# Kernel optimization log

Hardware: AMD Instinct MI355X
Metric: run time of the kernel (lower is better)

The kernel has to match this reference:

```python
import jax, jax.numpy as jnp
from jax import lax
import numpy as np

H = 512       # nhidden
IN = 300      # title/body input dim
TLEN = 40     # title_len
BLEN = 200    # body_len
B = 256       # batch
CH = 512      # classify_hidden
NC = 4        # nclass


def setup_inputs():
    key = jax.random.key(0)
    ks = jax.random.split(key, 17)
    s = 1.0 / np.sqrt(H)
    u = lambda k, sh: jax.random.uniform(k, sh, jnp.float32, -s, s)
    return {
        "x": jax.random.normal(ks[0], (B, TLEN + BLEN, IN), jnp.float32),
        "title_Wih": u(ks[1], (2, 4 * H, IN)),
        "title_Whh": u(ks[2], (2, 4 * H, H)),
        "title_bih": u(ks[3], (2, 4 * H)),
        "title_bhh": u(ks[4], (2, 4 * H)),
        "body_Wih": u(ks[5], (2, 4 * H, IN)),
        "body_Whh": u(ks[6], (2, 4 * H, H)),
        "body_bih": u(ks[7], (2, 4 * H)),
        "body_bhh": u(ks[8], (2, 4 * H)),
        "bil_W": u(ks[9], (1, 2 * H, 2 * H)),
        "bil_b": u(ks[10], (1,)),
        "attn_W": u(ks[11], (2 * H, 4 * H)),
        "attn_b": u(ks[12], (2 * H,)),
        "dec_W": u(ks[13], (CH, 4 * H)),
        "dec_b": u(ks[14], (CH,)),
        "cls_W": u(ks[15], (NC, CH)),
        "cls_b": u(ks[16], (NC,)),
    }


def _lstm_dir(x, Wih, Whh, bih, bhh, h0, c0, reverse):
    # x: [B, T, I]; precompute input-to-gate contributions for all timesteps
    xg = jnp.einsum('bti,gi->btg', x, Wih) + bih + bhh  # [B, T, 4H]

    def step(carry, xg_t):
        h, c = carry
        g = xg_t + h @ Whh.T  # PyTorch gate order: i, f, g, o
        i, f, gg, o = jnp.split(g, 4, axis=-1)
        c = jax.nn.sigmoid(f) * c + jax.nn.sigmoid(i) * jnp.tanh(gg)
        h = jax.nn.sigmoid(o) * jnp.tanh(c)
        return (h, c), h

    (hT, cT), hs = lax.scan(step, (h0, c0), jnp.swapaxes(xg, 0, 1), reverse=reverse)
    return jnp.swapaxes(hs, 0, 1), hT, cT  # outputs aligned to input time order


def _bilstm(x, Wih, Whh, bih, bhh, h0, c0):
    # h0, c0: [2, B, H] (dir 0 = forward, dir 1 = backward)
    out_f, hf, cf = _lstm_dir(x, Wih[0], Whh[0], bih[0], bhh[0], h0[0], c0[0], False)
    out_b, hb, cb = _lstm_dir(x, Wih[1], Whh[1], bih[1], bhh[1], h0[1], c0[1], True)
    out = jnp.concatenate([out_f, out_b], axis=-1)  # [B, T, 2H]
    return out, jnp.stack([hf, hb]), jnp.stack([cf, cb])


def reference(x, title_Wih, title_Whh, title_bih, title_bhh,
              body_Wih, body_Whh, body_bih, body_bhh,
              bil_W, bil_b, attn_W, attn_b, dec_W, dec_b, cls_W, cls_b):
    title, body = x[:, :TLEN, :], x[:, TLEN:, :]
    z = jnp.zeros((2, x.shape[0], H), x.dtype)
    title_out, hn, cn = _bilstm(title, title_Wih, title_Whh, title_bih, title_bhh, z, z)
    # conditional=True: body RNN starts from title final (h, c)
    body_out, _, _ = _bilstm(body, body_Wih, body_Whh, body_bih, body_bhh, hn, cn)
    body_last = body_out[:, -1, :]  # [B, 2H]
    # vectorized bilinear attention over title timesteps (replaces per-t loop)
    scores = jnp.einsum('bte,oeh,bh->bto', title_out, bil_W, body_last) + bil_b
    scores = jax.nn.softmax(scores[..., 0], axis=-1)  # [B, TLEN]
    context = jnp.einsum('bte,bt->be', title_out, scores)  # [B, 2H]
    attn = jnp.tanh(jnp.concatenate([context, body_last], axis=1) @ attn_W.T + attn_b)
    output = jnp.concatenate([title_out[:, -1, :], attn], axis=1)  # [B, 4H]
    class_hidden = output @ dec_W.T + dec_b  # dropout p=0.0 -> identity
    return jax.nn.softmax(class_hidden @ cls_W.T + cls_b, axis=-1)
```

## Files before the change

kernel.cpp:

```cpp
#include <hip/hip_runtime.h>
#include <math.h>

#define HD    512
#define BATCH 256
#define TDIM  240
#define INDIM 300

typedef unsigned short u16;
typedef u16   u16x8 __attribute__((ext_vector_type(8)));
typedef float f32x4 __attribute__((ext_vector_type(4)));

__device__ __forceinline__ u16 bf16_rte(float v) {
    unsigned u = __builtin_bit_cast(unsigned, v);
    unsigned r = (u + 0x7FFFu + ((u >> 16) & 1u)) >> 16;
    return (u16)r;
}

__device__ __forceinline__ void mfma16(f32x4& d, u16x8 a, u16x8 b) {
    asm("v_mfma_f32_16x16x32_bf16 %0, %1, %2, %0" : "+v"(d) : "v"(a), "v"(b));
}

__global__ __launch_bounds__(256) void split_pad(
    const float* __restrict__ src, u16* __restrict__ hi, u16* __restrict__ lo,
    int rows, int kin, int kout)
{
    long i = (long)blockIdx.x * 256 + threadIdx.x;
    if (i >= (long)rows * kout) return;
    int r = (int)(i / kout);
    int k = (int)(i - (long)r * kout);
    float v = (k < kin) ? src[(long)r * kin + k] : 0.f;
    u16 h = bf16_rte(v);
    float hf = __builtin_bit_cast(float, (unsigned)h << 16);
    hi[i] = h;
    lo[i] = bf16_rte(v - hf);
}

struct StepDir {
    const u16* Wih_h; const u16* Wih_l;
    const u16* Whh_h; const u16* Whh_l;
    const float* bih; const float* bhh;
    const u16* hh; const u16* hl;
    u16* oh; u16* ol;
    float* c;
    float* ex; long exs;
    int t;
};

__global__ __launch_bounds__(64) void step_mfma(
    const u16* __restrict__ xh, const u16* __restrict__ xl,
    StepDir d0, StepDir d1)
{
    StepDir D = blockIdx.z ? d1 : d0;
    const int gx   = blockIdx.x;
    const int xcd  = gx & 7, j = gx >> 3;
    const int cblk = xcd * 4 + (j & 3);
    const int rblk = j >> 2;
    const int lane = threadIdx.x;
    const int lr   = lane & 15;
    const int lk8  = (lane >> 4) * 8;
    const int b0   = rblk * 32;
    const int col  = cblk * 16 + lr;

    f32x4 acc[2][4];
    #pragma unroll
    for (int g = 0; g < 4; ++g) {
        float bs = D.bih[g * HD + col] + D.bhh[g * HD + col];
        acc[0][g] = f32x4{bs, bs, bs, bs};
// ... 60 lines not shown
        for (int ks = 0; ks < 16; ks += 2) {
            LD(Ah1, Al1, Bh1, Bl1, ks + 1);
            MMA(Ah0, Al0, Bh0, Bl0);
            if (ks + 2 < 16) LD(Ah0, Al0, Bh0, Bl0, ks + 2);
            MMA(Ah1, Al1, Bh1, Bl1);
        }
    }

    #pragma unroll
    for (int rt = 0; rt < 2; ++rt) {
        #pragma unroll
        for (int r = 0; r < 4; ++r) {
            const int b = b0 + rt * 16 + (lane >> 4) * 4 + r;
            const long hoff = (long)b * HD + col;
            float iv = acc[rt][0][r];
            float fv = acc[rt][1][r];
            float gv = acc[rt][2][r];
            float ov = acc[rt][3][r];
            float cp = D.c[hoff];
            float si = 1.f / (1.f + expf(-iv));
            float sf = 1.f / (1.f + expf(-fv));
            float so = 1.f / (1.f + expf(-ov));
            float cn = sf * cp + si * tanhf(gv);
            float hn = so * tanhf(cn);
            D.c[hoff] = cn;
            u16 hb = bf16_rte(hn);
            D.oh[hoff] = hb;
            D.ol[hoff] = bf16_rte(hn - __builtin_bit_cast(float, (unsigned)hb << 16));
            if (D.ex) D.ex[(long)b * D.exs + col] = hn;
        }
    }
}

__global__ __launch_bounds__(64) void xg_mfma(
    const u16* __restrict__ xh, const u16* __restrict__ xl,
    const u16* __restrict__ Wih_h, const u16* __restrict__ Wih_l,
    const float* __restrict__ bih, const float* __restrict__ bhh,
    float* __restrict__ xgT, int t0abs, int tstep)
{
    const int bx   = blockIdx.x;
    const int tloc = bx >> 9;
    const int rem  = bx & 511;
    const int rblk = rem >> 6;
    const int cgrp = rem & 63;
    const int lane = threadIdx.x;
    const int lr = lane & 15, lk8 = (lane >> 4) * 8;
    const int b0 = rblk * 32;
    const int tx = t0abs + tstep * tloc;
    const int colf0 = cgrp * 32 + lr;
    const int colf1 = colf0 + 16;

    f32x4 acc[2][2];
    {
        float bs0 = bih[colf0] + bhh[colf0];
        float bs1 = bih[colf1] + bhh[colf1];
        acc[0][0] = f32x4{bs0, bs0, bs0, bs0};
        acc[1][0] = f32x4{bs0, bs0, bs0, bs0};
        acc[0][1] = f32x4{bs1, bs1, bs1, bs1};
        acc[1][1] = f32x4{bs1, bs1, bs1, bs1};
    }

    u16x8 a0h[2], a0l[2], b0h[2], b0l[2];
    u16x8 a1h[2], a1l[2], b1h[2], b1l[2];

    auto LD = [&](u16x8 (&Ah)[2], u16x8 (&Al)[2], u16x8 (&Bh)[2], u16x8 (&Bl)[2], int ks) {
        const int ko = ks * 32 + lk8;
        #pragma unroll
        for (int rt = 0; rt < 2; ++rt) {
            long off = ((long)(b0 + rt * 16 + lr) * TDIM + tx) * 320 + ko;
            Ah[rt] = *(const u16x8*)(xh + off);
            Al[rt] = *(const u16x8*)(xl + off);
        }
        long w0 = (long)colf0 * 320 + ko;
        long w1 = (long)colf1 * 320 + ko;
        Bh[0] = *(const u16x8*)(Wih_h + w0);
        Bl[0] = *(const u16x8*)(Wih_l + w0);
        Bh[1] = *(const u16x8*)(Wih_h + w1);
        Bl[1] = *(const u16x8*)(Wih_l + w1);
    };
    auto MMA = [&](u16x8 (&Ah)[2], u16x8 (&Al)[2], u16x8 (&Bh)[2], u16x8 (&Bl)[2]) {
        #pragma unroll
        for (int rt = 0; rt < 2; ++rt)
            #pragma unroll
            for (int cf = 0; cf < 2; ++cf) {
                mfma16(acc[rt][cf], Ah[rt], Bh[cf]);
                mfma16(acc[rt][cf], Ah[rt], Bl[cf]);
                mfma16(acc[rt][cf], Al[rt], Bh[cf]);
            }
    };

    LD(a0h, a0l, b0h, b0l, 0);
    #pragma unroll
    for (int ks = 0; ks < 10; ks += 2) {
        LD(a1h, a1l, b1h, b1l, ks + 1);
        MMA(a0h, a0l, b0h, b0l);
        if (ks + 2 < 10) LD(a0h, a0l, b0h, b0l, ks + 2);
        MMA(a1h, a1l, b1h, b1l);
    }

    #pragma unroll
    for (int rt = 0; rt < 2; ++rt) {
        long o0 = ((long)tloc * 2048 + colf0) * 256 + b0 + rt * 16 + (lane >> 4) * 4;
        long o1 = ((long)tloc * 2048 + colf1) * 256 + b0 + rt * 16 + (lane >> 4) * 4;
        *(f32x4*)(xgT + o0) = acc[rt][0];
        *(f32x4*)(xgT + o1) = acc[rt][1];
    }
}

__device__ __forceinline__ void group_bar(unsigned* cnt, unsigned* gen,
                                          unsigned nb, unsigned g)
{
    __syncthreads();
    if (threadIdx.x == 0) {
        unsigned old = __hip_atomic_fetch_add(cnt, 1u, __ATOMIC_RELEASE,
                                              __HIP_MEMORY_SCOPE_AGENT);
        if (old == nb - 1u) {
            __hip_atomic_store(cnt, 0u, __ATOMIC_RELAXED, __HIP_MEMORY_SCOPE_AGENT);
            __hip_atomic_store(gen, g + 1u, __ATOMIC_RELEASE, __HIP_MEMORY_SCOPE_AGENT);
        } else {
            while (__hip_atomic_load(gen, __ATOMIC_RELAXED, __HIP_MEMORY_SCOPE_AGENT) < g + 1u)
                __builtin_amdgcn_s_sleep(2);
            (void)__hip_atomic_load(gen, __ATOMIC_ACQUIRE, __HIP_MEMORY_SCOPE_AGENT);
        }
    }
    __syncthreads();
}

struct ChainDirP {
    const u16* Whh_h; const u16* Whh_l;
    u16* hAh; u16* hAl; u16* hBh; u16* hBl;
    float* cst;
    float* ex; long ex_bstride;
    int ex_t0, ex_tstep, ex_coff, ex_final;
};

__global__ __launch_bounds__(256) void lstm_persist(
    const float* __restrict__ xgT,
    const u16* __restrict__ Whh_h, const u16* __restrict__ Whh_l,
    u16* __restrict__ hAh, u16* __restrict__ hAl,
    u16* __restrict__ hBh, u16* __restrict__ hBl,
    float* __restrict__ cst,
    float* __restrict__ ex, long ex_bstride, int ex_t0, int ex_tstep,
    int ex_coff, int ex_final,
    unsigned* __restrict__ bars, int s0, int L)
{
    const int gx   = blockIdx.x;
    const int rblk = gx & 7;
    const int cblk = gx >> 3;
    const int wid  = threadIdx.x >> 6;
    const int lane = threadIdx.x & 63;
    const int lr   = lane & 15;
    const int lk8  = (lane >> 4) * 8;
    const int b0   = rblk * 32;
    const int col  = cblk * 16 + lr;

    __shared__ u16 WH[64][520];
    __shared__ u16 WL[64][520];
    __shared__ f32x4 RED[3][64][8];

    for (int idx = threadIdx.x; idx < 64 * 64; idx += 256) {
        int rr = idx >> 6;
        int kk = (idx & 63) << 3;
        int g = rr >> 4, cc = rr & 15;
        long gro = (long)(g * HD + cblk * 16 + cc) * HD + kk;
        *(u16x8*)&WH[rr][kk] = *(const u16x8*)(Whh_h + gro);
        *(u16x8*)&WL[rr][kk] = *(const u16x8*)(Whh_l + gro);
    }
    __syncthreads();

    unsigned* bcnt = bars + rblk * 64;
    unsigned* bgen = bars + 512 + rblk * 64;
    unsigned gen = 0;
    const int ksbase = wid * 4;

    for (int ti = 0; ti < L; ++ti) {
        const int s = s0 + ti;
        const u16* hih = (s & 1) ? hBh : hAh;
        const u16* hil = (s & 1) ? hBl : hAl;
        u16* hoh = (s & 1) ? hAh : hBh;
        u16* hol = (s & 1) ? hAl : hBl;

        f32x4 acc[2][4];
        if (wid == 0) {
            #pragma unroll
            for (int rt = 0; rt < 2; ++rt)
                #pragma unroll
                for (int g = 0; g < 4; ++g) {
                    long o = ((long)ti * 2048 + g * HD + col) * 256
                             + b0 + rt * 16 + (lane >> 4) * 4;
                    acc[rt][g] = __builtin_nontemporal_load((const f32x4*)(xgT + o));
                }
        } else {
            #pragma unroll
            for (int rt = 0; rt < 2; ++rt)
                #pragma unroll
                for (int g = 0; g < 4; ++g) acc[rt][g] = f32x4{0.f, 0.f, 0.f, 0.f};
        }

        u16x8 Ah0[2], Al0[2], Bh0[4], Bl0[4];
        u16x8 Ah1[2], Al1[2], Bh1[4], Bl1[4];

        auto MMA = [&](u16x8 (&Ah)[2], u16x8 (&Al)[2], u16x8 (&Bh)[4], u16x8 (&Bl)[4]) {
            #pragma unroll
            for (int rt = 0; rt < 2; ++rt)
                #pragma unroll
                for (int g = 0; g < 4; ++g) {
                    mfma16(acc[rt][g], Ah[rt], Bh[g]);
                    mfma16(acc[rt][g], Ah[rt], Bl[g]);
                    mfma16(acc[rt][g], Al[rt], Bh[g]);
                }
        };
        auto LD = [&](u16x8 (&Ah)[2], u16x8 (&Al)[2], u16x8 (&Bh)[4], u16x8 (&Bl)[4], int ks) {
            const int ko = ks * 32 + lk8;
            #pragma unroll
            for (int rt = 0; rt < 2; ++rt) {
                long off = (long)(b0 + rt * 16 + lr) * HD + ko;
                Ah[rt] = *(const u16x8*)(hih + off);
                Al[rt] = *(const u16x8*)(hil + off);
            }
            #pragma unroll
            for (int g = 0; g < 4; ++g) {
                Bh[g] = *(const u16x8*)&WH[g * 16 + lr][ko];
                Bl[g] = *(const u16x8*)&WL[g * 16 + lr][ko];
            }
        };

        LD(Ah0, Al0, Bh0, Bl0, ksbase + 0);
        LD(Ah1, Al1, Bh1, Bl1, ksbase + 1);
        MMA(Ah0, Al0, Bh0, Bl0);
        LD(Ah0, Al0, Bh0, Bl0, ksbase + 2);
        MMA(Ah1, Al1, Bh1, Bl1);
        LD(Ah1, Al1, Bh1, Bl1, ksbase + 3);
        MMA(Ah0, Al0, Bh0, Bl0);
        MMA(Ah1, Al1, Bh1, Bl1);

        if (wid != 0) {
            #pragma unroll
            for (int rt = 0; rt < 2; ++rt)
                #pragma unroll
                for (int g = 0; g < 4; ++g)
                    RED[wid - 1][lane][rt * 4 + g] = acc[rt][g];
        }
        __syncthreads();

        if (wid == 0) {
            #pragma unroll
            for (int w = 0; w < 3; ++w)
                #pragma unroll
                for (int rt = 0; rt < 2; ++rt)
                    #pragma unroll
                    for (int g = 0; g < 4; ++g)
                        acc[rt][g] += RED[w][lane][rt * 4 + g];

            const bool exw = (ex_final == -2) || (ex_final >= 0 && ti == ex_final);
            const int tt = ex_t0 + ex_tstep * ti;
            #pragma unroll
            for (int rt = 0; rt < 2; ++rt) {
                #pragma unroll
                for (int r = 0; r < 4; ++r) {
                    const int b = b0 + rt * 16 + (lane >> 4) * 4 + r;
                    const long hoff = (long)b * HD + col;
                    float iv = acc[rt][0][r];
                    float fv = acc[rt][1][r];
                    float gv = acc[rt][2][r];
                    float ov = acc[rt][3][r];
                    float cp = cst[hoff];
                    float si = 1.f / (1.f + expf(-iv));
                    float sf = 1.f / (1.f + expf(-fv));
                    float so = 1.f / (1.f + expf(-ov));
                    float cn = sf * cp + si * tanhf(gv);
                    float hn = so * tanhf(cn);
                    cst[hoff] = cn;
                    u16 hb = bf16_rte(hn);
                    hoh[hoff] = hb;
                    hol[hoff] = bf16_rte(hn - __builtin_bit_cast(float, (unsigned)hb << 16));
                    if (exw) ex[(long)b * ex_bstride + (long)tt * 1024 + ex_coff + col] = hn;
                }
            }
        }
        if (ti + 1 < L) { group_bar(bcnt, bgen, 32u, gen); ++gen; }
    }
}

__global__ __launch_bounds__(64) void body_persist(
    const u16* __restrict__ xh, const u16* __restrict__ xl,
    const u16* __restrict__ Wih_h, const u16* __restrict__ Wih_l,
    const u16* __restrict__ Whh_h, const u16* __restrict__ Whh_l,
    const float* __restrict__ bih, const float* __restrict__ bhh,
    u16* __restrict__ hAh, u16* __restrict__ hAl,
    u16* __restrict__ hBh, u16* __restrict__ hBl,
    float* __restrict__ cst, float* __restrict__ ex,
    unsigned* __restrict__ bars)
{
    const int gx   = blockIdx.x;
    const int xcd  = gx & 7, j = gx >> 3;
    const int cblk = xcd * 4 + (j & 3);
    const int rblk = j >> 2;
    const int lane = threadIdx.x;
    const int lr   = lane & 15;
    const int lk8  = (lane >> 4) * 8;
    const int b0   = rblk * 32;
    const int col  = cblk * 16 + lr;

    __shared__ u16 WH[64][520];
    __shared__ u16 WL[64][520];
    for (int idx = lane; idx < 64 * 64; idx += 64) {
        int rr = idx >> 6;
        int kk = (idx & 63) << 3;
        int g = rr >> 4, cc = rr & 15;
        long gro = (long)(g * HD + cblk * 16 + cc) * HD + kk;
        *(u16x8*)&WH[rr][kk] = *(const u16x8*)(Whh_h + gro);
// ... 448 lines not shown
    float* c0 = (float*)carve(BATCH*HD*4);
    float* c1 = (float*)carve(BATCH*HD*4);
    unsigned* bars = (unsigned*)carve(32*4096);
    size_t zero_bytes = off;
    u16* hB0h = (u16*)carve(BATCH*HD*2);
    u16* hB0l = (u16*)carve(BATCH*HD*2);
    u16* hB1h = (u16*)carve(BATCH*HD*2);
    u16* hB1l = (u16*)carve(BATCH*HD*2);
    u16* xh = (u16*)carve((size_t)BATCH*TDIM*320*2);
    u16* xl = (u16*)carve((size_t)BATCH*TDIM*320*2);
    u16* tW0ih_h = (u16*)carve(2048*320*2); u16* tW0ih_l = (u16*)carve(2048*320*2);
    u16* tW1ih_h = (u16*)carve(2048*320*2); u16* tW1ih_l = (u16*)carve(2048*320*2);
    u16* bW0ih_h = (u16*)carve(2048*320*2); u16* bW0ih_l = (u16*)carve(2048*320*2);
    u16* bW1ih_h = (u16*)carve(2048*320*2); u16* bW1ih_l = (u16*)carve(2048*320*2);
    u16* tW0hh_h = (u16*)carve(2048*512*2); u16* tW0hh_l = (u16*)carve(2048*512*2);
    u16* tW1hh_h = (u16*)carve(2048*512*2); u16* tW1hh_l = (u16*)carve(2048*512*2);
    u16* bW0hh_h = (u16*)carve(2048*512*2); u16* bW0hh_l = (u16*)carve(2048*512*2);
    u16* bW1hh_h = (u16*)carve(2048*512*2); u16* bW1hh_l = (u16*)carve(2048*512*2);
    float* title_out = (float*)carve((size_t)BATCH*40*1024*4);
    float* body_last = (float*)carve((size_t)BATCH*1024*4);
    float* u_buf     = (float*)carve((size_t)BATCH*1024*4);
    float* attn_in   = (float*)carve((size_t)BATCH*2048*4);
    float* out_cat   = (float*)carve((size_t)BATCH*2048*4);
    float* ch        = (float*)carve((size_t)BATCH*512*4);
    u16* bl_h = (u16*)carve((size_t)BATCH*1024*2); u16* bl_l = (u16*)carve((size_t)BATCH*1024*2);
    u16* ai_h = (u16*)carve((size_t)BATCH*2048*2); u16* ai_l = (u16*)carve((size_t)BATCH*2048*2);
    u16* oc_h = (u16*)carve((size_t)BATCH*2048*2); u16* oc_l = (u16*)carve((size_t)BATCH*2048*2);
    u16* bilW_h  = (u16*)carve(1024*1024*2); u16* bilW_l  = (u16*)carve(1024*1024*2);
    u16* attnW_h = (u16*)carve((size_t)1024*2048*2); u16* attnW_l = (u16*)carve((size_t)1024*2048*2);
    u16* decW_h  = (u16*)carve((size_t)512*2048*2);  u16* decW_l  = (u16*)carve((size_t)512*2048*2);
    size_t need = off;

    const size_t SLAB_BYTES = (size_t)2048 * 256 * 4;
    float* xgT = (float*)(base + off);
    int C = 0;
    if (ws_size > need) {
        size_t nslab = (ws_size - need) / SLAB_BYTES;
        C = (int)(nslab > 50 ? 50 : nslab);
    }
    const bool xg_ok = (C >= 10);

    if (ws_size >= need) {
        hipMemsetAsync(d_ws, 0, zero_bytes, stream);

        auto SPLIT = [&](const float* s, u16* h, u16* l, long rows, int kin, int kout) {
            long n = rows * (long)kout;
            split_pad<<<dim3((unsigned)((n + 255) / 256)), 256, 0, stream>>>(s, h, l, (int)rows, kin, kout);
        };
        SPLIT(x, xh, xl, (long)BATCH*TDIM, INDIM, 320);
        SPLIT(tWih,               tW0ih_h, tW0ih_l, 2048, INDIM, 320);
        SPLIT(tWih + 2048*INDIM,  tW1ih_h, tW1ih_l, 2048, INDIM, 320);
        SPLIT(bWih,               bW0ih_h, bW0ih_l, 2048, INDIM, 320);
        SPLIT(bWih + 2048*INDIM,  bW1ih_h, bW1ih_l, 2048, INDIM, 320);
        SPLIT(tWhh,               tW0hh_h, tW0hh_l, 2048, HD, HD);
        SPLIT(tWhh + 2048*HD,     tW1hh_h, tW1hh_l, 2048, HD, HD);
        SPLIT(bWhh,               bW0hh_h, bW0hh_l, 2048, HD, HD);
        SPLIT(bWhh + 2048*HD,     bW1hh_h, bW1hh_l, 2048, HD, HD);
        SPLIT(bilW,  bilW_h,  bilW_l,  1024, 1024, 1024);
        SPLIT(attnW, attnW_h, attnW_l, 1024, 2048, 2048);
        SPLIT(decW,  decW_h,  decW_l,  512,  2048, 2048);

        if (xg_ok) {
            int ci = 0;
            for (int tb = 0; tb < 40; tb += C, ++ci) {
                int L = (C < 40 - tb) ? C : (40 - tb);
                xg_mfma<<<dim3((unsigned)(L*512)), 64, 0, stream>>>(
                    xh, xl, tW0ih_h, tW0ih_l, tbih, tbhh, xgT, tb, 1);
                lstm_persist<<<dim3(256), 256, 0, stream>>>(
                    xgT, tW0hh_h, tW0hh_l, hA0h, hA0l, hB0h, hB0l, c0,
                    title_out, 40*1024, tb, 1, 0, -2,
                    bars + (size_t)ci*1024, tb, L);
            }
            for (int tb = 0; tb < 40; tb += C, ++ci) {
                int L = (C < 40 - tb) ? C : (40 - tb);
                xg_mfma<<<dim3((unsigned)(L*512)), 64, 0, stream>>>(
                    xh, xl, tW1ih_h, tW1ih_l, tbih + 2048, tbhh + 2048, xgT, 39 - tb, -1);
                lstm_persist<<<dim3(256), 256, 0, stream>>>(
                    xgT, tW1hh_h, tW1hh_l, hA1h, hA1l, hB1h, hB1l, c1,
                    title_out, 40*1024, 39 - tb, -1, 512, -2,
                    bars + (size_t)ci*1024, tb, L);
            }
            {
                StepDir F = { bW0ih_h, bW0ih_l, bW0hh_h, bW0hh_l, bbih, bbhh,
                              hA0h, hA0l, hB0h, hB0l, c0, (float*)nullptr, 0, 40 };
                StepDir R = { bW1ih_h, bW1ih_l, bW1hh_h, bW1hh_l, bbih + 2048, bbhh + 2048,
                              hA1h, hA1l, hB1h, hB1l, c1, body_last + 512, 1024, 239 };
                step_mfma<<<dim3(256,1,2), 64, 0, stream>>>(xh, xl, F, R);
            }
            for (int tb = 1; tb < 200; tb += C, ++ci) {
                int L = (C < 200 - tb) ? C : (200 - tb);
                bool last = (tb + L == 200);
                xg_mfma<<<dim3((unsigned)(L*512)), 64, 0, stream>>>(
                    xh, xl, bW0ih_h, bW0ih_l, bbih, bbhh, xgT, 40 + tb, 1);
                lstm_persist<<<dim3(256), 256, 0, stream>>>(
                    xgT, bW0hh_h, bW0hh_l, hA0h, hA0l, hB0h, hB0l, c0,
                    body_last, 1024, 0, 0, 0, last ? (L - 1) : -1,
                    bars + (size_t)ci*1024, 40 + tb, L);
            }
        } else {
            for (int t = 0; t < 40; ++t) {
                bool odd = t & 1;
                StepDir A = { tW0ih_h, tW0ih_l, tW0hh_h, tW0hh_l, tbih, tbhh,
                              odd?hB0h:hA0h, odd?hB0l:hA0l, odd?hA0h:hB0h, odd?hA0l:hB0l,
                              c0, title_out + (size_t)t*1024, 40*1024, t };
                StepDir B = { tW1ih_h, tW1ih_l, tW1hh_h, tW1hh_l, tbih + 2048, tbhh + 2048,
                              odd?hB1h:hA1h, odd?hB1l:hA1l, odd?hA1h:hB1h, odd?hA1l:hB1l,
                              c1, title_out + (size_t)(39 - t)*1024 + 512, 40*1024, 39 - t };
                step_mfma<<<dim3(256,1,2), 64, 0, stream>>>(xh, xl, A, B);
            }
            {
                StepDir F = { bW0ih_h, bW0ih_l, bW0hh_h, bW0hh_l, bbih, bbhh,
                              hA0h, hA0l, hB0h, hB0l, c0, (float*)nullptr, 0, 40 };
                StepDir R = { bW1ih_h, bW1ih_l, bW1hh_h, bW1hh_l, bbih + 2048, bbhh + 2048,
                              hA1h, hA1l, hB1h, hB1l, c1, body_last + 512, 1024, 239 };
                step_mfma<<<dim3(256,1,2), 64, 0, stream>>>(xh, xl, F, R);
            }
            body_persist<<<dim3(256), 64, 0, stream>>>(
                xh, xl, bW0ih_h, bW0ih_l, bW0hh_h, bW0hh_l, bbih, bbhh,
                hA0h, hA0l, hB0h, hB0l, c0, body_last, bars);
        }

        SPLIT(body_last, bl_h, bl_l, 256, 1024, 1024);
        mfma_gemm<0><<<dim3(8*64), 64, 0, stream>>>(bl_h, bl_l, bilW_h, bilW_l,
                                                    (const float*)nullptr, u_buf, 1024, 1024, 64);
        attn_ctx<<<256, 256, 0, stream>>>(title_out, u_buf, bilb, attn_in);
        copy_rows<<<256, 256, 0, stream>>>(body_last, 1024, attn_in + 1024, 2048, 1024);
        copy_rows<<<256, 256, 0, stream>>>(title_out + 39*1024, 40*1024, out_cat, 2048, 1024);
        SPLIT(attn_in, ai_h, ai_l, 256, 2048, 2048);
        mfma_gemm<1><<<dim3(8*64), 64, 0, stream>>>(ai_h, ai_l, attnW_h, attnW_l,
                                                    attnb, out_cat + 1024, 2048, 2048, 64);
        SPLIT(out_cat, oc_h, oc_l, 256, 2048, 2048);
        mfma_gemm<0><<<dim3(8*32), 64, 0, stream>>>(oc_h, oc_l, decW_h, decW_l,
                                                    decb, ch, 512, 2048, 32);
        final_cls<<<4, 64, 0, stream>>>(ch, clsW, clsb, (float*)d_out);
    } else {
        float* p = (float*)d_ws;
        float* lhA0 = p; p += BATCH*HD;
        float* lc0  = p; p += BATCH*HD;
        float* lhA1 = p; p += BATCH*HD;
        float* lc1  = p; p += BATCH*HD;
        float* lhB0 = p; p += BATCH*HD;
        float* lhB1 = p; p += BATCH*HD;
        float* l_title = p; p += (size_t)BATCH*40*1024;
        float* l_blast = p; p += BATCH*1024;
        float* l_u     = p; p += BATCH*1024;
        float* l_ain   = p; p += BATCH*2048;
        float* l_ocat  = p; p += BATCH*2048;
        float* l_ch    = p; p += BATCH*512;

        hipMemsetAsync(lhA0, 0, (size_t)4*BATCH*HD*sizeof(float), stream);
        const float* tWih1 = tWih + 2048*INDIM;
        const float* tWhh1 = tWhh + 2048*HD;
        const float* bWih1 = bWih + 2048*INDIM;
        const float* bWhh1 = bWhh + 2048*HD;

        for (int t = 0; t < 40; ++t) {
            float* hi0 = (t & 1) ? lhB0 : lhA0;
            float* ho0 = (t & 1) ? lhA0 : lhB0;
            float* hi1 = (t & 1) ? lhB1 : lhA1;
            float* ho1 = (t & 1) ? lhA1 : lhB1;
            lstm_step<64><<<dim3(4,32,2), 256, 0, stream>>>(
                x, tWih, tWhh, tbih, tbhh, hi0, ho0, lc0,
                l_title + t*1024, 40*1024, t,
                tWih1, tWhh1, tbih + 2048, tbhh + 2048, hi1, ho1, lc1,
// ... 25 lines not shown
```

Before: 4.872 ms.

## Overlap next chunk's input-gate GEMM with recurrent LSTM steps in persistent kernel

The persistent LSTM kernel now launches 512 threads per block. Four waves run the recurrent step as before, and four extra waves compute the input-gate projections (xg) for the next time chunk into a double-buffered workspace. This removes the separate xg_mfma launches between chunks and hides that GEMM behind the latency-bound recurrence. The costs are a halved chunk length (C) because the workspace is split into two buffers, more launches overall, and possible contention for memory bandwidth and CUs with the critical-path recurrent waves.

```diff
diff --git a/kernel.cpp b/kernel.cpp
--- a/kernel.cpp
+++ b/kernel.cpp
@@ -159,18 +159,17 @@
     }
 }
 
-__global__ __launch_bounds__(64) void xg_mfma(
+__device__ __forceinline__ void xg_job(
+    int bx, int lane,
     const u16* __restrict__ xh, const u16* __restrict__ xl,
     const u16* __restrict__ Wih_h, const u16* __restrict__ Wih_l,
     const float* __restrict__ bih, const float* __restrict__ bhh,
     float* __restrict__ xgT, int t0abs, int tstep)
 {
-    const int bx   = blockIdx.x;
     const int tloc = bx >> 9;
     const int rem  = bx & 511;
     const int rblk = rem >> 6;
     const int cgrp = rem & 63;
-    const int lane = threadIdx.x;
     const int lr = lane & 15, lk8 = (lane >> 4) * 8;
     const int b0 = rblk * 32;
     const int tx = t0abs + tstep * tloc;
@@ -232,6 +231,15 @@
         *(f32x4*)(xgT + o0) = acc[rt][0];
         *(f32x4*)(xgT + o1) = acc[rt][1];
     }
+}
+
+__global__ __launch_bounds__(64) void xg_mfma(
+    const u16* __restrict__ xh, const u16* __restrict__ xl,
+    const u16* __restrict__ Wih_h, const u16* __restrict__ Wih_l,
+    const float* __restrict__ bih, const float* __restrict__ bhh,
+    float* __restrict__ xgT, int t0abs, int tstep)
+{
+    xg_job(blockIdx.x, threadIdx.x, xh, xl, Wih_h, Wih_l, bih, bhh, xgT, t0abs, tstep);
 }
 
 __device__ __forceinline__ void group_bar(unsigned* cnt, unsigned* gen,
@@ -253,15 +261,13 @@
     __syncthreads();
 }
 
-struct ChainDirP {
-    const u16* Whh_h; const u16* Whh_l;
-    u16* hAh; u16* hAl; u16* hBh; u16* hBl;
-    float* cst;
-    float* ex; long ex_bstride;
-    int ex_t0, ex_tstep, ex_coff, ex_final;
+struct NextXG {
+    const u16* Wih_h; const u16* Wih_l;
+    const float* bih; const float* bhh;
+    float* dst; int t0abs; int tstep; int L;
 };
 
-__global__ __launch_bounds__(256) void lstm_persist(
+__global__ __launch_bounds__(512) void lstm_persist(
     const float* __restrict__ xgT,
     const u16* __restrict__ Whh_h, const u16* __restrict__ Whh_l,
     u16* __restrict__ hAh, u16* __restrict__ hAl,
@@ -269,7 +275,9 @@
     float* __restrict__ cst,
     float* __restrict__ ex, long ex_bstride, int ex_t0, int ex_tstep,
     int ex_coff, int ex_final,
-    unsigned* __restrict__ bars, int s0, int L)
+    unsigned* __restrict__ bars, int s0, int L,
+    const u16* __restrict__ xh, const u16* __restrict__ xl,
+    NextXG nx)
 {
     const int gx   = blockIdx.x;
     const int rblk = gx & 7;
@@ -285,7 +293,7 @@
     __shared__ u16 WL[64][520];
     __shared__ f32x4 RED[3][64][8];
 
-    for (int idx = threadIdx.x; idx < 64 * 64; idx += 256) {
+    for (int idx = threadIdx.x; idx < 64 * 64; idx += 512) {
         int rr = idx >> 6;
         int kk = (idx & 63) << 3;
         int g = rr >> 4, cc = rr & 15;
@@ -298,7 +306,11 @@
     unsigned* bcnt = bars + rblk * 64;
     unsigned* bgen = bars + 512 + rblk * 64;
     unsigned gen = 0;
-    const int ksbase = wid * 4;
+    const int ksbase = (wid & 3) * 4;
+
+    const long Jtot = (long)nx.L * 512;
+    const int q = (nx.L > 0) ? (int)((Jtot + (long)1024 * L - 1) / ((long)1024 * L)) : 0;
+    long jidx = (long)gx * 4 + (wid - 4);
 
     for (int ti = 0; ti < L; ++ti) {
         const int s = s0 + ti;
@@ -308,65 +320,76 @@
         u16* hol = (s & 1) ? hAl : hBl;
 
         f32x4 acc[2][4];
-        if (wid == 0) {
-            #pragma unroll
-            for (int rt = 0; rt < 2; ++rt)
+        if (wid < 4) {
+            if (wid == 0) {
+                #pragma unroll
+                for (int rt = 0; rt < 2; ++rt)
+                    #pragma unroll
+                    for (int g = 0; g < 4; ++g) {
+                        long o = ((long)ti * 2048 + g * HD + col) * 256
+                                 + b0 + rt * 16 + (lane >> 4) * 4;
+                        acc[rt][g] = __builtin_nontemporal_load((const f32x4*)(xgT + o));
+                    }
+            } else {
+                #pragma unroll
+                for (int rt = 0; rt < 2; ++rt)
+                    #pragma unroll
+                    for (int g = 0; g < 4; ++g) acc[rt][g] = f32x4{0.f, 0.f, 0.f, 0.f};
+            }
+
+            u16x8 Ah0[2], Al0[2], Bh0[4], Bl0[4];
+            u16x8 Ah1[2], Al1[2], Bh1[4], Bl1[4];
+
+            auto MMA = [&](u16x8 (&Ah)[2], u16x8 (&Al)[2], u16x8 (&Bh)[4], u16x8 (&Bl)[4]) {
+                #pragma unroll
+                for (int rt = 0; rt < 2; ++rt)
+                    #pragma unroll
+                    for (int g = 0; g < 4; ++g) {
+                        mfma16(acc[rt][g], Ah[rt], Bh[g]);
+                        mfma16(acc[rt][g], Ah[rt], Bl[g]);
+                        mfma16(acc[rt][g], Al[rt], Bh[g]);
+                    }
+            };
+            auto LD = [&](u16x8 (&Ah)[2], u16x8 (&Al)[2], u16x8 (&Bh)[4], u16x8 (&Bl)[4], int ks) {
+                const int ko = ks * 32 + lk8;
+                #pragma unroll
+                for (int rt = 0; rt < 2; ++rt) {
+                    long off = (long)(b0 + rt * 16 + lr) * HD + ko;
+                    Ah[rt] = *(const u16x8*)(hih + off);
+                    Al[rt] = *(const u16x8*)(hil + off);
+                }
                 #pragma unroll
                 for (int g = 0; g < 4; ++g) {
-                    long o = ((long)ti * 2048 + g * HD + col) * 256
-                             + b0 + rt * 16 + (lane >> 4) * 4;
-                    acc[rt][g] = __builtin_nontemporal_load((const f32x4*)(xgT + o));
+                    Bh[g] = *(const u16x8*)&WH[g * 16 + lr][ko];
+                    Bl[g] = *(const u16x8*)&WL[g * 16 + lr][ko];
                 }
+            };
+
+            LD(Ah0, Al0, Bh0, Bl0, ksbase + 0);
+            LD(Ah1, Al1, Bh1, Bl1, ksbase + 1);
+            MMA(Ah0, Al0, Bh0, Bl0);
+            LD(Ah0, Al0, Bh0, Bl0, ksbase + 2);
+            MMA(Ah1, Al1, Bh1, Bl1);
+            LD(Ah1, Al1, Bh1, Bl1, ksbase + 3);
+            MMA(Ah0, Al0, Bh0, Bl0);
+            MMA(Ah1, Al1, Bh1, Bl1);
+
+            if (wid != 0) {
+                #pragma unroll
+                for (int rt = 0; rt < 2; ++rt)
+                    #pragma unroll
+                    for (int g = 0; g < 4; ++g)
+                        RED[wid - 1][lane][rt * 4 + g] = acc[rt][g];
+            }
         } else {
-            #pragma unroll
-            for (int rt = 0; rt < 2; ++rt)
-                #pragma unroll
-                for (int g = 0; g < 4; ++g) acc[rt][g] = f32x4{0.f, 0.f, 0.f, 0.f};
-        }
-
-        u16x8 Ah0[2], Al0[2], Bh0[4], Bl0[4];
-        u16x8 Ah1[2], Al1[2], Bh1[4], Bl1[4];
-
-        auto MMA = [&](u16x8 (&Ah)[2], u16x8 (&Al)[2], u16x8 (&Bh)[4], u16x8 (&Bl)[4]) {
-            #pragma unroll
-            for (int rt = 0; rt < 2; ++rt)
-                #pragma unroll
-                for (int g = 0; g < 4; ++g) {
-                    mfma16(acc[rt][g], Ah[rt], Bh[g]);
-                    mfma16(acc[rt][g], Ah[rt], Bl[g]);
-                    mfma16(acc[rt][g], Al[rt], Bh[g]);
+            #pragma unroll 1
+            for (int itq = 0; itq < q; ++itq) {
+                if (jidx < Jtot) {
+                    xg_job((int)jidx, lane, xh, xl, nx.Wih_h, nx.Wih_l,
+                           nx.bih, nx.bhh, nx.dst, nx.t0abs, nx.tstep);
+                    jidx += 1024;
                 }
-        };
-        auto LD = [&](u16x8 (&Ah)[2], u16x8 (&Al)[2], u16x8 (&Bh)[4], u16x8 (&Bl)[4], int ks) {
-            const int ko = ks * 32 + lk8;
-            #pragma unroll
-            for (int rt = 0; rt < 2; ++rt) {
-                long off = (long)(b0 + rt * 16 + lr) * HD + ko;
-                Ah[rt] = *(const u16x8*)(hih + off);
-                Al[rt] = *(const u16x8*)(hil + off);
-            }
-            #pragma unroll
-            for (int g = 0; g < 4; ++g) {
-                Bh[g] = *(const u16x8*)&WH[g * 16 + lr][ko];
-                Bl[g] = *(const u16x8*)&WL[g * 16 + lr][ko];
-            }
-        };
-
-        LD(Ah0, Al0, Bh0, Bl0, ksbase + 0);
-        LD(Ah1, Al1, Bh1, Bl1, ksbase + 1);
-        MMA(Ah0, Al0, Bh0, Bl0);
-        LD(Ah0, Al0, Bh0, Bl0, ksbase + 2);
-        MMA(Ah1, Al1, Bh1, Bl1);
-        LD(Ah1, Al1, Bh1, Bl1, ksbase + 3);
-        MMA(Ah0, Al0, Bh0, Bl0);
-        MMA(Ah1, Al1, Bh1, Bl1);
-
-        if (wid != 0) {
-            #pragma unroll
-            for (int rt = 0; rt < 2; ++rt)
-                #pragma unroll
-                for (int g = 0; g < 4; ++g)
-                    RED[wid - 1][lane][rt * 4 + g] = acc[rt][g];
+            }
         }
         __syncthreads();
 
@@ -918,13 +941,16 @@
     size_t need = off;
 
     const size_t SLAB_BYTES = (size_t)2048 * 256 * 4;
-    float* xgT = (float*)(base + off);
+    float* xgBase = (float*)(base + off);
     int C = 0;
     if (ws_size > need) {
         size_t nslab = (ws_size - need) / SLAB_BYTES;
-        C = (int)(nslab > 50 ? 50 : nslab);
+        size_t half = nslab / 2;
+        C = (int)(half > 50 ? 50 : half);
     }
     const bool xg_ok = (C >= 10);
+    const long SLABF = 2048L * 256;
+    auto buf = [&](int i) { return xgBase + (size_t)(i & 1) * C * SLABF; };
 
     if (ws_size >= need) {
         hipMemsetAsync(d_ws, 0, zero_bytes, stream);
@@ -947,41 +973,56 @@
         SPLIT(decW,  decW_h,  decW_l,  512,  2048, 2048);
 
         if (xg_ok) {
-            int ci = 0;
-            for (int tb = 0; tb < 40; tb += C, ++ci) {
+            struct PD {
+                NextXG xg;
+                const u16 *Whh_h, *Whh_l;
+                u16 *hAh, *hAl, *hBh, *hBl;
+                float* cst;
+                float* ex; long exb; int ext0, extstep, excoff, exfinal;
+                int s0, L;
+            };
+            PD d[32]; int nd = 0;
+            for (int tb = 0; tb < 40; tb += C) {
                 int L = (C < 40 - tb) ? C : (40 - tb);
-                xg_mfma<<<dim3((unsigned)(L*512)), 64, 0, stream>>>(
-                    xh, xl, tW0ih_h, tW0ih_l, tbih, tbhh, xgT, tb, 1);
-                lstm_persist<<<dim3(256), 256, 0, stream>>>(
-                    xgT, tW0hh_h, tW0hh_l, hA0h, hA0l, hB0h, hB0l, c0,
-                    title_out, 40*1024, tb, 1, 0, -2,
-                    bars + (size_t)ci*1024, tb, L);
-            }
-            for (int tb = 0; tb < 40; tb += C, ++ci) {
+                d[nd++] = { { tW0ih_h, tW0ih_l, tbih, tbhh, nullptr, tb, 1, L },
+                            tW0hh_h, tW0hh_l, hA0h, hA0l, hB0h, hB0l, c0,
+                            title_out, 40*1024, tb, 1, 0, -2, tb, L };
+            }
+            for (int tb = 0; tb < 40; tb += C) {
                 int L = (C < 40 - tb) ? C : (40 - tb);
-                xg_mfma<<<dim3((unsigned)(L*512)), 64, 0, stream>>>(
-                    xh, xl, tW1ih_h, tW1ih_l, tbih + 2048, tbhh + 2048, xgT, 39 - tb, -1);
-                lstm_persist<<<dim3(256), 256, 0, stream>>>(
-                    xgT, tW1hh_h, tW1hh_l, hA1h, hA1l, hB1h, hB1l, c1,
-                    title_out, 40*1024, 39 - tb, -1, 512, -2,
-                    bars + (size_t)ci*1024, tb, L);
-            }
-            {
-                StepDir F = { bW0ih_h, bW0ih_l, bW0hh_h, bW0hh_l, bbih, bbhh,
-                              hA0h, hA0l, hB0h, hB0l, c0, (float*)nullptr, 0, 40 };
-                StepDir R = { bW1ih_h, bW1ih_l, bW1hh_h, bW1hh_l, bbih + 2048, bbhh + 2048,
-                              hA1h, hA1l, hB1h, hB1l, c1, body_last + 512, 1024, 239 };
-                step_mfma<<<dim3(256,1,2), 64, 0, stream>>>(xh, xl, F, R);
-            }
-            for (int tb = 1; tb < 200; tb += C, ++ci) {
+                d[nd++] = { { tW1ih_h, tW1ih_l, tbih + 2048, tbhh + 2048, nullptr, 39 - tb, -1, L },
+                            tW1hh_h, tW1hh_l, hA1h, hA1l, hB1h, hB1l, c1,
+                            title_out, 40*1024, 39 - tb, -1, 512, -2, tb, L };
+            }
+            const int body_idx = nd;
+            for (int tb = 1; tb < 200; tb += C) {
                 int L = (C < 200 - tb) ? C : (200 - tb);
                 bool last = (tb + L == 200);
-                xg_mfma<<<dim3((unsigned)(L*512)), 64, 0, stream>>>(
-                    xh, xl, bW0ih_h, bW0ih_l, bbih, bbhh, xgT, 40 + tb, 1);
-                lstm_persist<<<dim3(256), 256, 0, stream>>>(
-                    xgT, bW0hh_h, bW0hh_l, hA0h, hA0l, hB0h, hB0l, c0,
-                    body_last, 1024, 0, 0, 0, last ? (L - 1) : -1,
-                    bars + (size_t)ci*1024, 40 + tb, L);
+                d[nd++] = { { bW0ih_h, bW0ih_l, bbih, bbhh, nullptr, 40 + tb, 1, L },
+                            bW0hh_h, bW0hh_l, hA0h, hA0l, hB0h, hB0l, c0,
+                            body_last, 1024, 0, 0, 0, last ? (L - 1) : -1, 40 + tb, L };
+            }
+
+            xg_mfma<<<dim3((unsigned)(d[0].xg.L * 512)), 64, 0, stream>>>(
+                xh, xl, d[0].xg.Wih_h, d[0].xg.Wih_l, d[0].xg.bih, d[0].xg.bhh,
+                buf(0), d[0].xg.t0abs, d[0].xg.tstep);
+
+            for (int i = 0; i < nd; ++i) {
+                if (i == body_idx) {
+                    StepDir F = { bW0ih_h, bW0ih_l, bW0hh_h, bW0hh_l, bbih, bbhh,
+                                  hA0h, hA0l, hB0h, hB0l, c0, (float*)nullptr, 0, 40 };
+                    StepDir R = { bW1ih_h, bW1ih_l, bW1hh_h, bW1hh_l, bbih + 2048, bbhh + 2048,
+                                  hA1h, hA1l, hB1h, hB1l, c1, body_last + 512, 1024, 239 };
+                    step_mfma<<<dim3(256,1,2), 64, 0, stream>>>(xh, xl, F, R);
+                }
+                NextXG nx = { nullptr, nullptr, nullptr, nullptr, nullptr, 0, 0, 0 };
+                if (i + 1 < nd) { nx = d[i + 1].xg; nx.dst = buf(i + 1); }
+                lstm_persist<<<dim3(256), 512, 0, stream>>>(
+                    buf(i), d[i].Whh_h, d[i].Whh_l,
+                    d[i].hAh, d[i].hAl, d[i].hBh, d[i].hBl, d[i].cst,
+                    d[i].ex, d[i].exb, d[i].ext0, d[i].extstep, d[i].excoff, d[i].exfinal,
+                    bars + (size_t)i * 1024, d[i].s0, d[i].L,
+                    xh, xl, nx);
             }
         } else {
             for (int t = 0; t < 40; ++t) {
```

After: 5.371 ms. +10.2%, slower.

## Run both title LSTM directions concurrently in one persistent kernel; batch weight splits

Applied to the files above, without the earlier changes.

Adds a dual-direction persistent LSTM kernel for the title pass, where block groups 0-3 run the forward direction and 4-7 the backward direction, each covering 64 batch rows per block in two halves. The two directions are no longer run one after the other. Precomputed input gates for both directions go into adjacent workspace slabs. It also merges the twelve bf16 hi/lo weight-split launches into a single split_all kernel with a job table to cut launch overhead. The cost is that each block does twice the batch work per step, and the new path needs enough workspace for paired slabs.

```diff
diff --git a/kernel.cpp b/kernel.cpp
--- a/kernel.cpp
+++ b/kernel.cpp
@@ -33,6 +33,27 @@
     float hf = __builtin_bit_cast(float, (unsigned)h << 16);
     hi[i] = h;
     lo[i] = bf16_rte(v - hf);
+}
+
+struct SJob { const float* src; u16* hi; u16* lo; int kin; int kout; };
+struct SParams { SJob j[12]; long cum[13]; };
+
+__global__ __launch_bounds__(256) void split_all(SParams P)
+{
+    long gid = (long)blockIdx.x * 256 + threadIdx.x;
+    if (gid >= P.cum[12]) return;
+    int sgi = 0;
+    #pragma unroll
+    for (int k = 1; k < 12; ++k) if (gid >= P.cum[k]) sgi = k;
+    const SJob& J = P.j[sgi];
+    long i = gid - P.cum[sgi];
+    int r = (int)(i / J.kout);
+    int k = (int)(i - (long)r * J.kout);
+    float v = (k < J.kin) ? J.src[(long)r * J.kin + k] : 0.f;
+    u16 h = bf16_rte(v);
+    float hf = __builtin_bit_cast(float, (unsigned)h << 16);
+    J.hi[i] = h;
+    J.lo[i] = bf16_rte(v - hf);
 }
 
 struct StepDir {
@@ -253,14 +274,6 @@
     __syncthreads();
 }
 
-struct ChainDirP {
-    const u16* Whh_h; const u16* Whh_l;
-    u16* hAh; u16* hAl; u16* hBh; u16* hBl;
-    float* cst;
-    float* ex; long ex_bstride;
-    int ex_t0, ex_tstep, ex_coff, ex_final;
-};
-
 __global__ __launch_bounds__(256) void lstm_persist(
     const float* __restrict__ xgT,
     const u16* __restrict__ Whh_h, const u16* __restrict__ Whh_l,
@@ -404,6 +417,165 @@
                     if (exw) ex[(long)b * ex_bstride + (long)tt * 1024 + ex_coff + col] = hn;
                 }
             }
+        }
+        if (ti + 1 < L) { group_bar(bcnt, bgen, 32u, gen); ++gen; }
+    }
+}
+
+struct DualDir {
+    const u16* Whh_h; const u16* Whh_l;
+    u16 *hAh, *hAl, *hBh, *hBl;
+    float* cst;
+    float* ex; long exb; int ext0, extstep, excoff;
+};
+
+__global__ __launch_bounds__(256) void lstm_persist_dual(
+    const float* __restrict__ xgT, long dirStride,
+    DualDir d0, DualDir d1,
+    unsigned* __restrict__ bars, int s0, int L)
+{
+    const int gx   = blockIdx.x;
+    const int grp  = gx & 7;
+    const int dir  = grp >> 2;
+    const int rb2  = grp & 3;
+    const int cblk = gx >> 3;
+    const int wid  = threadIdx.x >> 6;
+    const int lane = threadIdx.x & 63;
+    const int lr   = lane & 15;
+    const int lk8  = (lane >> 4) * 8;
+    const int col  = cblk * 16 + lr;
+
+    const DualDir D = dir ? d1 : d0;
+    const float* xgD = xgT + (dir ? dirStride : 0);
+
+    __shared__ u16 WH[64][520];
+    __shared__ u16 WL[64][520];
+    __shared__ f32x4 RED[3][64][8];
+
+    for (int idx = threadIdx.x; idx < 64 * 64; idx += 256) {
+        int rr = idx >> 6;
+        int kk = (idx & 63) << 3;
+        int g = rr >> 4, cc = rr & 15;
+        long gro = (long)(g * HD + cblk * 16 + cc) * HD + kk;
+        *(u16x8*)&WH[rr][kk] = *(const u16x8*)(D.Whh_h + gro);
+        *(u16x8*)&WL[rr][kk] = *(const u16x8*)(D.Whh_l + gro);
+    }
+    __syncthreads();
+
+    unsigned* bcnt = bars + grp * 64;
+    unsigned* bgen = bars + 512 + grp * 64;
+    unsigned gen = 0;
+    const int ksbase = wid * 4;
+
+    for (int ti = 0; ti < L; ++ti) {
+        const int s = s0 + ti;
+        const u16* hih = (s & 1) ? D.hBh : D.hAh;
+        const u16* hil = (s & 1) ? D.hBl : D.hAl;
+        u16* hoh = (s & 1) ? D.hAh : D.hBh;
+        u16* hol = (s & 1) ? D.hAl : D.hBl;
+
+        #pragma unroll
+        for (int t2 = 0; t2 < 2; ++t2) {
+            const int b0 = rb2 * 64 + t2 * 32;
+
+            f32x4 acc[2][4];
+            if (wid == 0) {
+                #pragma unroll
+                for (int rt = 0; rt < 2; ++rt)
+                    #pragma unroll
+                    for (int g = 0; g < 4; ++g) {
+                        long o = ((long)ti * 2048 + g * HD + col) * 256
+                                 + b0 + rt * 16 + (lane >> 4) * 4;
+                        acc[rt][g] = __builtin_nontemporal_load((const f32x4*)(xgD + o));
+                    }
+            } else {
+                #pragma unroll
+                for (int rt = 0; rt < 2; ++rt)
+                    #pragma unroll
+                    for (int g = 0; g < 4; ++g) acc[rt][g] = f32x4{0.f, 0.f, 0.f, 0.f};
+            }
+
+            u16x8 Ah0[2], Al0[2], Bh0[4], Bl0[4];
+            u16x8 Ah1[2], Al1[2], Bh1[4], Bl1[4];
+
+            auto MMA = [&](u16x8 (&Ah)[2], u16x8 (&Al)[2], u16x8 (&Bh)[4], u16x8 (&Bl)[4]) {
+                #pragma unroll
+                for (int rt = 0; rt < 2; ++rt)
+                    #pragma unroll
+                    for (int g = 0; g < 4; ++g) {
+                        mfma16(acc[rt][g], Ah[rt], Bh[g]);
+                        mfma16(acc[rt][g], Ah[rt], Bl[g]);
+                        mfma16(acc[rt][g], Al[rt], Bh[g]);
+                    }
+            };
+            auto LD = [&](u16x8 (&Ah)[2], u16x8 (&Al)[2], u16x8 (&Bh)[4], u16x8 (&Bl)[4], int ks) {
+                const int ko = ks * 32 + lk8;
+                #pragma unroll
+                for (int rt = 0; rt < 2; ++rt) {
+                    long off = (long)(b0 + rt * 16 + lr) * HD + ko;
+                    Ah[rt] = *(const u16x8*)(hih + off);
+                    Al[rt] = *(const u16x8*)(hil + off);
+                }
+                #pragma unroll
+                for (int g = 0; g < 4; ++g) {
+                    Bh[g] = *(const u16x8*)&WH[g * 16 + lr][ko];
+                    Bl[g] = *(const u16x8*)&WL[g * 16 + lr][ko];
+                }
+            };
+
+            LD(Ah0, Al0, Bh0, Bl0, ksbase + 0);
+            LD(Ah1, Al1, Bh1, Bl1, ksbase + 1);
+            MMA(Ah0, Al0, Bh0, Bl0);
+            LD(Ah0, Al0, Bh0, Bl0, ksbase + 2);
+            MMA(Ah1, Al1, Bh1, Bl1);
+            LD(Ah1, Al1, Bh1, Bl1, ksbase + 3);
+            MMA(Ah0, Al0, Bh0, Bl0);
+            MMA(Ah1, Al1, Bh1, Bl1);
+
+            if (wid != 0) {
+                #pragma unroll
+                for (int rt = 0; rt < 2; ++rt)
+                    #pragma unroll
+                    for (int g = 0; g < 4; ++g)
+                        RED[wid - 1][lane][rt * 4 + g] = acc[rt][g];
+            }
+            __syncthreads();
+
+            if (wid == 0) {
+                #pragma unroll
+                for (int w = 0; w < 3; ++w)
+                    #pragma unroll
+                    for (int rt = 0; rt < 2; ++rt)
+                        #pragma unroll
+                        for (int g = 0; g < 4; ++g)
+                            acc[rt][g] += RED[w][lane][rt * 4 + g];
+
+                const int tt = D.ext0 + D.extstep * ti;
+                #pragma unroll
+                for (int rt = 0; rt < 2; ++rt) {
+                    #pragma unroll
+                    for (int r = 0; r < 4; ++r) {
+                        const int b = b0 + rt * 16 + (lane >> 4) * 4 + r;
+                        const long hoff = (long)b * HD + col;
+                        float iv = acc[rt][0][r];
+                        float fv = acc[rt][1][r];
+                        float gv = acc[rt][2][r];
+                        float ov = acc[rt][3][r];
+                        float cp = D.cst[hoff];
+                        float si = 1.f / (1.f + expf(-iv));
+                        float sf = 1.f / (1.f + expf(-fv));
+                        float so = 1.f / (1.f + expf(-ov));
+                        float cn = sf * cp + si * tanhf(gv);
+                        float hn = so * tanhf(cn);
+                        D.cst[hoff] = cn;
+                        u16 hb = bf16_rte(hn);
+                        hoh[hoff] = hb;
+                        hol[hoff] = bf16_rte(hn - __builtin_bit_cast(float, (unsigned)hb << 16));
+                        D.ex[(long)b * D.exb + (long)tt * 1024 + D.excoff + col] = hn;
+                    }
+                }
+            }
+            __syncthreads();
         }
         if (ti + 1 < L) { group_bar(bcnt, bgen, 32u, gen); ++gen; }
     }
@@ -918,53 +1090,78 @@
     size_t need = off;
 
     const size_t SLAB_BYTES = (size_t)2048 * 256 * 4;
+    const long   SLABF = 2048L * 256;
     float* xgT = (float*)(base + off);
-    int C = 0;
-    if (ws_size > need) {
-        size_t nslab = (ws_size - need) / SLAB_BYTES;
-        C = (int)(nslab > 50 ? 50 : nslab);
-    }
+    size_t nslab = 0;
+    if (ws_size > need) nslab = (ws_size - need) / SLAB_BYTES;
+    int C = (int)(nslab > 50 ? 50 : nslab);
     const bool xg_ok = (C >= 10);
+    int C2 = (int)(nslab / 2 > 40 ? 40 : nslab / 2);
+    const bool dual_ok = (C2 >= 10);
 
     if (ws_size >= need) {
         hipMemsetAsync(d_ws, 0, zero_bytes, stream);
 
-        auto SPLIT = [&](const float* s, u16* h, u16* l, long rows, int kin, int kout) {
-            long n = rows * (long)kout;
-            split_pad<<<dim3((unsigned)((n + 255) / 256)), 256, 0, stream>>>(s, h, l, (int)rows, kin, kout);
-        };
-        SPLIT(x, xh, xl, (long)BATCH*TDIM, INDIM, 320);
-        SPLIT(tWih,               tW0ih_h, tW0ih_l, 2048, INDIM, 320);
-        SPLIT(tWih + 2048*INDIM,  tW1ih_h, tW1ih_l, 2048, INDIM, 320);
-        SPLIT(bWih,               bW0ih_h, bW0ih_l, 2048, INDIM, 320);
-        SPLIT(bWih + 2048*INDIM,  bW1ih_h, bW1ih_l, 2048, INDIM, 320);
-        SPLIT(tWhh,               tW0hh_h, tW0hh_l, 2048, HD, HD);
-        SPLIT(tWhh + 2048*HD,     tW1hh_h, tW1hh_l, 2048, HD, HD);
-        SPLIT(bWhh,               bW0hh_h, bW0hh_l, 2048, HD, HD);
-        SPLIT(bWhh + 2048*HD,     bW1hh_h, bW1hh_l, 2048, HD, HD);
-        SPLIT(bilW,  bilW_h,  bilW_l,  1024, 1024, 1024);
-        SPLIT(attnW, attnW_h, attnW_l, 1024, 2048, 2048);
-        SPLIT(decW,  decW_h,  decW_l,  512,  2048, 2048);
+        {
+            SParams P;
+            auto J = [&](int i, const float* s, u16* h, u16* l, long rows, int kin, int kout) {
+                P.j[i] = { s, h, l, kin, kout };
+                P.cum[i + 1] = P.cum[i] + rows * (long)kout;
+            };
+            P.cum[0] = 0;
+            J(0,  x,                  xh,      xl,      (long)BATCH*TDIM, INDIM, 320);
+            J(1,  tWih,               tW0ih_h, tW0ih_l, 2048, INDIM, 320);
+            J(2,  tWih + 2048*INDIM,  tW1ih_h, tW1ih_l, 2048, INDIM, 320);
+            J(3,  bWih,               bW0ih_h, bW0ih_l, 2048, INDIM, 320);
+            J(4,  bWih + 2048*INDIM,  bW1ih_h, bW1ih_l, 2048, INDIM, 320);
+            J(5,  tWhh,               tW0hh_h, tW0hh_l, 2048, HD, HD);
+            J(6,  tWhh + 2048*HD,     tW1hh_h, tW1hh_l, 2048, HD, HD);
+            J(7,  bWhh,               bW0hh_h, bW0hh_l, 2048, HD, HD);
+            J(8,  bWhh + 2048*HD,     bW1hh_h, bW1hh_l, 2048, HD, HD);
+            J(9,  bilW,               bilW_h,  bilW_l,  1024, 1024, 1024);
+            J(10, attnW,              attnW_h, attnW_l, 1024, 2048, 2048);
+            J(11, decW,               decW_h,  decW_l,  512,  2048, 2048);
+            long total = P.cum[12];
+            split_all<<<dim3((unsigned)((total + 255) / 256)), 256, 0, stream>>>(P);
+        }
 
         if (xg_ok) {
             int ci = 0;
-            for (int tb = 0; tb < 40; tb += C, ++ci) {
-                int L = (C < 40 - tb) ? C : (40 - tb);
-                xg_mfma<<<dim3((unsigned)(L*512)), 64, 0, stream>>>(
-                    xh, xl, tW0ih_h, tW0ih_l, tbih, tbhh, xgT, tb, 1);
-                lstm_persist<<<dim3(256), 256, 0, stream>>>(
-                    xgT, tW0hh_h, tW0hh_l, hA0h, hA0l, hB0h, hB0l, c0,
-                    title_out, 40*1024, tb, 1, 0, -2,
-                    bars + (size_t)ci*1024, tb, L);
-            }
-            for (int tb = 0; tb < 40; tb += C, ++ci) {
-                int L = (C < 40 - tb) ? C : (40 - tb);
-                xg_mfma<<<dim3((unsigned)(L*512)), 64, 0, stream>>>(
-                    xh, xl, tW1ih_h, tW1ih_l, tbih + 2048, tbhh + 2048, xgT, 39 - tb, -1);
-                lstm_persist<<<dim3(256), 256, 0, stream>>>(
-                    xgT, tW1hh_h, tW1hh_l, hA1h, hA1l, hB1h, hB1l, c1,
-                    title_out, 40*1024, 39 - tb, -1, 512, -2,
-                    bars + (size_t)ci*1024, tb, L);
+            if (dual_ok) {
+                for (int tb = 0; tb < 40; tb += C2, ++ci) {
+                    int L = (C2 < 40 - tb) ? C2 : (40 - tb);
+                    xg_mfma<<<dim3((unsigned)(L*512)), 64, 0, stream>>>(
+                        xh, xl, tW0ih_h, tW0ih_l, tbih, tbhh, xgT, tb, 1);
+                    xg_mfma<<<dim3((unsigned)(L*512)), 64, 0, stream>>>(
+                        xh, xl, tW1ih_h, tW1ih_l, tbih + 2048, tbhh + 2048,
+                        xgT + (long)L * SLABF, 39 - tb, -1);
+                    DualDir D0 = { tW0hh_h, tW0hh_l, hA0h, hA0l, hB0h, hB0l, c0,
+                                   title_out, 40*1024, tb, 1, 0 };
+                    DualDir D1 = { tW1hh_h, tW1hh_l, hA1h, hA1l, hB1h, hB1l, c1,
+                                   title_out, 40*1024, 39 - tb, -1, 512 };
+                    lstm_persist_dual<<<dim3(256), 256, 0, stream>>>(
+                        xgT, (long)L * SLABF, D0, D1,
+                        bars + (size_t)ci*1024, tb, L);
+                }
+            } else {
+                for (int tb = 0; tb < 40; tb += C, ++ci) {
+                    int L = (C < 40 - tb) ? C : (40 - tb);
+                    xg_mfma<<<dim3((unsigned)(L*512)), 64, 0, stream>>>(
+                        xh, xl, tW0ih_h, tW0ih_l, tbih, tbhh, xgT, tb, 1);
+                    lstm_persist<<<dim3(256), 256, 0, stream>>>(
+                        xgT, tW0hh_h, tW0hh_l, hA0h, hA0l, hB0h, hB0l, c0,
+                        title_out, 40*1024, tb, 1, 0, -2,
+                        bars + (size_t)ci*1024, tb, L);
+                }
+                for (int tb = 0; tb < 40; tb += C, ++ci) {
+                    int L = (C < 40 - tb) ? C : (40 - tb);
+                    xg_mfma<<<dim3((unsigned)(L*512)), 64, 0, stream>>>(
+                        xh, xl, tW1ih_h, tW1ih_l, tbih + 2048, tbhh + 2048, xgT, 39 - tb, -1);
+                    lstm_persist<<<dim3(256), 256, 0, stream>>>(
+                        xgT, tW1hh_h, tW1hh_l, hA1h, hA1l, hB1h, hB1l, c1,
+                        title_out, 40*1024, 39 - tb, -1, 512, -2,
+                        bars + (size_t)ci*1024, tb, L);
+                }
             }
             {
                 StepDir F = { bW0ih_h, bW0ih_l, bW0hh_h, bW0hh_l, bbih, bbhh,
@@ -1006,16 +1203,19 @@
                 hA0h, hA0l, hB0h, hB0l, c0, body_last, bars);
         }
 
-        SPLIT(body_last, bl_h, bl_l, 256, 1024, 1024);
+        split_pad<<<dim3((unsigned)((256*1024 + 255)/256)), 256, 0, stream>>>(
+            body_last, bl_h, bl_l, 256, 1024, 1024);
         mfma_gemm<0><<<dim3(8*64), 64, 0, stream>>>(bl_h, bl_l, bilW_h, bilW_l,
                                                     (const float*)nullptr, u_buf, 1024, 1024, 64);
         attn_ctx<<<256, 256, 0, stream>>>(title_out, u_buf, bilb, attn_in);
         copy_rows<<<256, 256, 0, stream>>>(body_last, 1024, attn_in + 1024, 2048, 1024);
         copy_rows<<<256, 256, 0, stream>>>(title_out + 39*1024, 40*1024, out_cat, 2048, 1024);
-        SPLIT(attn_in, ai_h, ai_l, 256, 2048, 2048);
+        split_pad<<<dim3((unsigned)((256*2048 + 255)/256)), 256, 0, stream>>>(
+            attn_in, ai_h, ai_l, 256, 2048, 2048);
         mfma_gemm<1><<<dim3(8*64), 64, 0, stream>>>(ai_h, ai_l, attnW_h, attnW_l,
                                                     attnb, out_cat + 1024, 2048, 2048, 64);
-        SPLIT(out_cat, oc_h, oc_l, 256, 2048, 2048);
+        split_pad<<<dim3((unsigned)((256*2048 + 255)/256)), 256, 0, stream>>>(
+            out_cat, oc_h, oc_l, 256, 2048, 2048);
         mfma_gemm<0><<<dim3(8*32), 64, 0, stream>>>(oc_h, oc_l, decW_h, decW_l,
                                                     decb, ch, 512, 2048, 32);
         final_cls<<<4, 64, 0, stream>>>(ch, clsW, clsb, (float*)d_out);
```

After: 4.798 ms. About the same (-1.5%).
